# Performance work log

Hardware: AMD Instinct MI355X
Metric: run time of the kernel (lower is better)

Reference implementation:

```python
import jax, jax.numpy as jnp
import numpy as np

B, TQ, TV = 4, 256, 256
H, D, U = 512, 512, 256  # hidden_size, value_size, units


def setup_inputs() -> dict:
    key = jax.random.key(0)
    ks = jax.random.split(key, 8)
    s = 0.02
    return {
        "query": jax.random.normal(ks[0], (B, TQ, H), dtype=jnp.float32),
        "values": jax.random.normal(ks[1], (B, TV, D), dtype=jnp.float32),
        "W1": jax.random.normal(ks[2], (H, U), dtype=jnp.float32) * s,
        "b1": jnp.zeros((U,), dtype=jnp.float32),
        "W2": jax.random.normal(ks[3], (D, U), dtype=jnp.float32) * s,
        "b2": jnp.zeros((U,), dtype=jnp.float32),
        "V": jax.random.normal(ks[4], (U, 1), dtype=jnp.float32) * s,
        "bV": jnp.zeros((1,), dtype=jnp.float32),
    }


def reference(query, values, W1, b1, W2, b2, V, bV):
    # query: [B,Tq,H]  values: [B,Tv,D]
    q = jnp.einsum("bqh,hu->bqu", query, W1) + b1          # [B,Tq,U]
    v = jnp.einsum("bvd,du->bvu", values, W2) + b2          # [B,Tv,U]
    # tf.repeat over Tq is just a broadcast of v; same math without materializing repeats twice
    hidden = jnp.tanh(q[:, :, None, :] + v[:, None, :, :])  # [B,Tq,Tv,U]
    score = jnp.einsum("bqvu,u->bqv", hidden, V[:, 0]) + bV[0]  # [B,Tq,Tv]
    attn = jax.nn.softmax(score, axis=2)                    # softmax over Tv (axis=2 of score)
    context = jnp.einsum("bqv,bvd->bqd", attn, values)      # [B,Tq,D]
    return context, attn[..., None]                          # weights returned as [B,Tq,Tv,1] like TF
```

## Files before the change

### kernel.cpp

```cpp
#include <hip/hip_runtime.h>
#include <math.h>


typedef float f4 __attribute__((ext_vector_type(4)));
typedef float f2 __attribute__((ext_vector_type(2)));
typedef __attribute__((ext_vector_type(8))) short s8v;
typedef __attribute__((ext_vector_type(4))) unsigned short u4v;

#define B_    4
#define TQ_   256
#define TV_   256
#define D_    512
#define U_    256
#define KDIM  512
#define MROWS 1024

#define C2LOG2E 2.8853900817779268f

#define EQ_OFF  0
#define EVT_OFF 262144

#if __has_builtin(__builtin_amdgcn_exp2f)
#define EXP2F(x) __builtin_amdgcn_exp2f(x)
#else
#define EXP2F(x) exp2f(x)
#endif
#if __has_builtin(__builtin_amdgcn_rcpf)
#define RCPF(x) __builtin_amdgcn_rcpf(x)
#else
#define RCPF(x) (1.0f / (x))
#endif

__device__ __forceinline__ unsigned short f2bf(float f) {
    union { float f; unsigned u; } v; v.f = f;
    return (unsigned short)((v.u + 0x7FFF + ((v.u >> 16) & 1)) >> 16);
}

__global__ __launch_bounds__(256) void proj_mfma(
    const float* __restrict__ query, const float* __restrict__ values,
    const float* __restrict__ W1, const float* __restrict__ b1,
    const float* __restrict__ W2, const float* __restrict__ b2,
    float* __restrict__ ws)
{
    __shared__ unsigned short Al[2][32][40];
    __shared__ unsigned short Bl[2][32][40];

    const int tid  = threadIdx.x;
    const int proj = blockIdx.y;
    const int x    = blockIdx.x;

    int m0, n0;
    if (proj == 0) { m0 = (x >> 3) * 32; n0 = (x & 7) * 32; }
    else           { m0 = (x & 7) * 32;  n0 = (x >> 3) * 32; }

    const int drow = tid >> 3;
    const int dk   = (tid & 7) * 4;
    const int tcol = drow;
    const int tk   = dk;

    const float* dptr = (proj ? values + (size_t)(n0 + drow) * KDIM
                              : query  + (size_t)(m0 + drow) * KDIM) + dk;
    const float* tptr = (proj ? W2 + (m0 + tcol) : W1 + (n0 + tcol))
                        + (size_t)tk * U_;

    f4 d0;
    float tv0, tv1, tv2, tv3;

#define LOADR(S)                                                        \
    do {                                                                \
        d0 = *(const f4*)(dptr + (size_t)(S) * 32);                     \
        const float* tp = tptr + (size_t)(S) * 32 * U_;                 \
        tv0 = tp[0]; tv1 = tp[U_]; tv2 = tp[2 * U_]; tv3 = tp[3 * U_];  \
    } while (0)

#define WRITEB(BUF)                                                     \
    do {                                                                \
        u4v dd, tt;                                                     \
        dd[0] = f2bf(d0[0]); dd[1] = f2bf(d0[1]);                       \
        dd[2] = f2bf(d0[2]); dd[3] = f2bf(d0[3]);                       \
        tt[0] = f2bf(tv0);   tt[1] = f2bf(tv1);                         \
        tt[2] = f2bf(tv2);   tt[3] = f2bf(tv3);                         \
        unsigned short* ddst = proj ? &Bl[BUF][drow][dk] : &Al[BUF][drow][dk]; \
        unsigned short* tdst = proj ? &Al[BUF][tcol][tk] : &Bl[BUF][tcol][tk]; \
        *(u4v*)ddst = dd;                                               \
        *(u4v*)tdst = tt;                                               \
    } while (0)

    f4 acc = {};

    const int w    = tid >> 6;
    const int l    = tid & 63;
    const int fr   = l & 15;
    const int fk   = (l >> 4) * 8;
    const int band = (w & 1) * 16;
    const int colh = (w >> 1) * 16;

    LOADR(0);
    WRITEB(0);

    for (int s = 0; s < 16; ++s) {
        __syncthreads();
        if (s + 1 < 16) LOADR(s + 1);
        {
            const int bu = s & 1;
            s8v af = *(const s8v*)&Al[bu][band + fr][fk];
            s8v bf = *(const s8v*)&Bl[bu][colh + fr][fk];
            acc = __builtin_amdgcn_mfma_f32_16x16x32_bf16(af, bf, acc, 0, 0, 0);
        }
        if (s + 1 < 16) WRITEB((s + 1) & 1);
    }
#undef LOADR
#undef WRITEB

    const int orow = m0 + band + (l >> 4) * 4;
    const int ocol = n0 + colh + (l & 15);

    if (proj == 0) {
        float* E = ws + EQ_OFF;
        const float bias = b1[ocol];
        #pragma unroll
        for (int r = 0; r < 4; ++r)
            E[(size_t)(orow + r) * U_ + ocol] =
                EXP2F((acc[r] + bias) * C2LOG2E);
    } else {
        float* E = ws + EVT_OFF;
        #pragma unroll
        for (int r = 0; r < 4; ++r)
            E[(size_t)(orow + r) * MROWS + ocol] =
                EXP2F((acc[r] + b2[orow + r]) * C2LOG2E);
    }
}

__global__ __launch_bounds__(256) void score_softmax(
    const float* __restrict__ Vw, const float* __restrict__ ws,
    float* __restrict__ out)
{
    __shared__ float redmin[4][2];
    __shared__ float redsum[4][2];

    const int tid = threadIdx.x;
    const int b  = blockIdx.y;
    const int q0 = blockIdx.x * 2;

    const float* eq0 = ws + EQ_OFF + (size_t)(b * TQ_ + q0) * U_;
    const float* eq1 = eq0 + U_;
    const float* evp = ws + EVT_OFF + (size_t)b * TV_ + tid;
    float* attn = out + (size_t)B_ * TQ_ * D_ + (size_t)(b * TQ_ + q0) * TV_;

    float evA[8], evB[8];
    #pragma unroll
    for (int i = 0; i < 8; ++i) evA[i] = evp[(size_t)i * MROWS];

    f2 p = {0.f, 0.f};
    const f2 one = {1.0f, 1.0f};

#define SGRP(BUF, G)                                                    \
    _Pragma("unroll")                                                   \
    for (int i = 0; i < 8; ++i) {                                       \
        const int u = (G) * 8 + i;                                      \
        f2 eq = {eq0[u], eq1[u]};                      \
        f2 ev2 = {BUF[i], BUF[i]};                                      \
        f2 den = eq * ev2 + one;                      \
        f2 r = {RCPF(den.x), RCPF(den.y)};                              \
        f2 wv = {Vw[u], Vw[u]};                             \
        p = wv * r + p;                               \
    }

    #pragma unroll
    for (int g = 0; g < 32; g += 2) {
        #pragma unroll
        for (int i = 0; i < 8; ++i)
            evB[i] = evp[(size_t)((g + 1) * 8 + i) * MROWS];
        SGRP(evA, g)
        if (g + 2 < 32) {
            #pragma unroll
            for (int i = 0; i < 8; ++i)
                evA[i] = evp[(size_t)((g + 2) * 8 + i) * MROWS];
        }
        SGRP(evB, g + 1)
    }
#undef SGRP

    const int w = tid >> 6, lane = tid & 63;
    float m0 = p.x, m1 = p.y;
    #pragma unroll
    for (int off = 32; off; off >>= 1) {
        m0 = fminf(m0, __shfl_xor(m0, off));
        m1 = fminf(m1, __shfl_xor(m1, off));
    }
    if (lane == 0) { redmin[w][0] = m0; redmin[w][1] = m1; }
    __syncthreads();
    m0 = fminf(fminf(redmin[0][0], redmin[1][0]),
               fminf(redmin[2][0], redmin[3][0]));
    m1 = fminf(fminf(redmin[0][1], redmin[1][1]),
               fminf(redmin[2][1], redmin[3][1]));

    float e0 = EXP2F((m0 - p.x) * C2LOG2E);
    float e1 = EXP2F((m1 - p.y) * C2LOG2E);

    float s0 = e0, s1 = e1;
    #pragma unroll
    for (int off = 32; off; off >>= 1) {
        s0 += __shfl_xor(s0, off);
        s1 += __shfl_xor(s1, off);
    }
    if (lane == 0) { redsum[w][0] = s0; redsum[w][1] = s1; }
    __syncthreads();
    s0 = redsum[0][0] + redsum[1][0] + redsum[2][0] + redsum[3][0];
    s1 = redsum[0][1] + redsum[1][1] + redsum[2][1] + redsum[3][1];

    attn[tid]       = e0 * (1.0f / s0);
    attn[TV_ + tid] = e1 * (1.0f / s1);
}

__global__ __launch_bounds__(256) void ctx_mfma(
    const float* __restrict__ values, float* __restrict__ out)
{
    __shared__ unsigned short Al[2][32][40];
    __shared__ unsigned short Bl[2][32][40];

    const int tid = threadIdx.x;
    const int b   = blockIdx.y;
    const int x   = blockIdx.x;
    const int m0  = (x >> 4) * 32;
    const int n0  = (x & 15) * 32;

    const int drow = tid >> 3;
    const int dk   = (tid & 7) * 4;

    const float* attn = out + (size_t)B_ * TQ_ * D_ + (size_t)b * TQ_ * TV_;
    const float* valb = values + (size_t)b * TV_ * D_;

    const float* dptr = attn + (size_t)(m0 + drow) * TV_ + dk;
    const float* tptr = valb + (n0 + drow) + (size_t)dk * D_;

    f4 d0;
    float tv0, tv1, tv2, tv3;

#define LOADC(S)                                                        \
    do {                                                                \
        d0 = *(const f4*)(dptr + (size_t)(S) * 32);                     \
        const float* tp = tptr + (size_t)(S) * 32 * D_;                 \
        tv0 = tp[0]; tv1 = tp[D_]; tv2 = tp[2 * D_]; tv3 = tp[3 * D_];  \
    } while (0)

#define WRITEC(BUF)                                                     \
    do {                                                                \
        u4v dd, tt;                                                     \
        dd[0] = f2bf(d0[0]); dd[1] = f2bf(d0[1]);                       \
        dd[2] = f2bf(d0[2]); dd[3] = f2bf(d0[3]);                       \
        tt[0] = f2bf(tv0);   tt[1] = f2bf(tv1);                         \
        tt[2] = f2bf(tv2);   tt[3] = f2bf(tv3);                         \
        *(u4v*)&Al[BUF][drow][dk] = dd;                                 \
        *(u4v*)&Bl[BUF][drow][dk] = tt;                                 \
    } while (0)

    f4 acc = {};

    const int w    = tid >> 6;
    const int l    = tid & 63;
    const int fr   = l & 15;
    const int fk   = (l >> 4) * 8;
    const int band = (w & 1) * 16;
    const int colh = (w >> 1) * 16;

    LOADC(0);
    WRITEC(0);

    for (int s = 0; s < 8; ++s) {
        __syncthreads();
        if (s + 1 < 8) LOADC(s + 1);
        {
            const int bu = s & 1;
            s8v af = *(const s8v*)&Al[bu][band + fr][fk];
            s8v bf = *(const s8v*)&Bl[bu][colh + fr][fk];
            acc = __builtin_amdgcn_mfma_f32_16x16x32_bf16(af, bf, acc, 0, 0, 0);
        }
        if (s + 1 < 8) WRITEC((s + 1) & 1);
    }
#undef LOADC
#undef WRITEC

    const int orow = m0 + band + (l >> 4) * 4;
    const int ocol = n0 + colh + (l & 15);
    float* C = out + (size_t)b * TQ_ * D_;

    #pragma unroll
    for (int r = 0; r < 4; ++r)
        C[(size_t)(orow + r) * D_ + ocol] = acc[r];
}

extern "C" void kernel_launch(void* const* d_in, const int* in_sizes, int n_in,
                              void* d_out, int out_size, void* d_ws, size_t ws_size,
                              hipStream_t stream) {
    const float* query  = (const float*)d_in[0];
    const float* values = (const float*)d_in[1];
    const float* W1     = (const float*)d_in[2];
    const float* b1     = (const float*)d_in[3];
    const float* W2     = (const float*)d_in[4];
    const float* b2     = (const float*)d_in[5];
    const float* Vw     = (const float*)d_in[6];
    float* out = (float*)d_out;
    float* ws  = (float*)d_ws;

    proj_mfma<<<dim3(256, 2), 256, 0, stream>>>(query, values, W1, b1, W2, b2, ws);
    score_softmax<<<dim3(TQ_ / 2, B_), 256, 0, stream>>>(Vw, ws, out);
    ctx_mfma<<<dim3(128, B_), 256, 0, stream>>>(values, out);
}
```

Baseline: 40.78 us.

## Precompute bf16 transposed values and bf16 attention for context GEMM

Adds a third job to the projection kernel that writes values transposed into workspace as bf16. It also stores the exp(2v) projection as bf16, and has the softmax kernel write a bf16 copy of the attention weights. The context GEMM then loads contiguous 16-byte bf16 vectors with a 64-wide K step, instead of strided fp32 loads with per-element conversion. This removes uncoalesced column reads and conversion work from the context kernel, at the cost of extra workspace writes, an extra grid slice, and reduced precision on the exp(v) intermediate.

```diff
diff --git a/kernel.cpp b/kernel.cpp
--- a/kernel.cpp
+++ b/kernel.cpp
@@ -6,6 +6,7 @@
 typedef float f2 __attribute__((ext_vector_type(2)));
 typedef __attribute__((ext_vector_type(8))) short s8v;
 typedef __attribute__((ext_vector_type(4))) unsigned short u4v;
+typedef __attribute__((ext_vector_type(8))) unsigned short u8v;
 
 #define B_    4
 #define TQ_   256
@@ -17,8 +18,9 @@
 
 #define C2LOG2E 2.8853900817779268f
 
-#define EQ_OFF  0
-#define EVT_OFF 262144
+#define EVT_U16_OFF   524288
+#define ATTN_U16_OFF  786432
+#define VALT_U16_OFF 1048576
 
 #if __has_builtin(__builtin_amdgcn_exp2f)
 #define EXP2F(x) __builtin_amdgcn_exp2f(x)
@@ -35,6 +37,10 @@
     union { float f; unsigned u; } v; v.f = f;
     return (unsigned short)((v.u + 0x7FFF + ((v.u >> 16) & 1)) >> 16);
 }
+__device__ __forceinline__ float bf2f(unsigned short h) {
+    union { unsigned u; float f; } v; v.u = (unsigned)h << 16;
+    return v.f;
+}
 
 __global__ __launch_bounds__(256) void proj_mfma(
     const float* __restrict__ query, const float* __restrict__ values,
@@ -42,11 +48,27 @@
     const float* __restrict__ W2, const float* __restrict__ b2,
     float* __restrict__ ws)
 {
+    const int tid = threadIdx.x;
+    const int job = blockIdx.y;
+
+    if (job == 2) {
+        const int idx = blockIdx.x * 256 + tid;
+        const int d   = idx & 511;
+        const int vg  = (idx >> 9) & 31;
+        const int b   = idx >> 14;
+        const float* src = values + ((size_t)b * TV_ + vg * 8) * KDIM + d;
+        unsigned short* valT = (unsigned short*)ws + VALT_U16_OFF;
+        u8v o;
+        #pragma unroll
+        for (int j = 0; j < 8; ++j) o[j] = f2bf(src[(size_t)j * KDIM]);
+        *(u8v*)(valT + ((size_t)b * D_ + d) * TV_ + vg * 8) = o;
+        return;
+    }
+
     __shared__ unsigned short Al[2][32][40];
     __shared__ unsigned short Bl[2][32][40];
 
-    const int tid  = threadIdx.x;
-    const int proj = blockIdx.y;
+    const int proj = job;
     const int x    = blockIdx.x;
 
     int m0, n0;
@@ -116,23 +138,23 @@
     const int ocol = n0 + colh + (l & 15);
 
     if (proj == 0) {
-        float* E = ws + EQ_OFF;
+        float* E = ws;
         const float bias = b1[ocol];
         #pragma unroll
         for (int r = 0; r < 4; ++r)
             E[(size_t)(orow + r) * U_ + ocol] =
                 EXP2F((acc[r] + bias) * C2LOG2E);
     } else {
-        float* E = ws + EVT_OFF;
+        unsigned short* E = (unsigned short*)ws + EVT_U16_OFF;
         #pragma unroll
         for (int r = 0; r < 4; ++r)
             E[(size_t)(orow + r) * MROWS + ocol] =
-                EXP2F((acc[r] + b2[orow + r]) * C2LOG2E);
+                f2bf(EXP2F((acc[r] + b2[orow + r]) * C2LOG2E));
     }
 }
 
 __global__ __launch_bounds__(256) void score_softmax(
-    const float* __restrict__ Vw, const float* __restrict__ ws,
+    const float* __restrict__ Vw, float* __restrict__ ws,
     float* __restrict__ out)
 {
     __shared__ float redmin[4][2];
@@ -142,14 +164,17 @@
     const int b  = blockIdx.y;
     const int q0 = blockIdx.x * 2;
 
-    const float* eq0 = ws + EQ_OFF + (size_t)(b * TQ_ + q0) * U_;
+    const float* eq0 = ws + (size_t)(b * TQ_ + q0) * U_;
     const float* eq1 = eq0 + U_;
-    const float* evp = ws + EVT_OFF + (size_t)b * TV_ + tid;
+    const unsigned short* evp =
+        (const unsigned short*)ws + EVT_U16_OFF + (size_t)b * TV_ + tid;
     float* attn = out + (size_t)B_ * TQ_ * D_ + (size_t)(b * TQ_ + q0) * TV_;
+    unsigned short* attnbf =
+        (unsigned short*)ws + ATTN_U16_OFF + (size_t)(b * TQ_ + q0) * TV_;
 
     float evA[8], evB[8];
     #pragma unroll
-    for (int i = 0; i < 8; ++i) evA[i] = evp[(size_t)i * MROWS];
+    for (int i = 0; i < 8; ++i) evA[i] = bf2f(evp[(size_t)i * MROWS]);
 
     f2 p = {0.f, 0.f};
     const f2 one = {1.0f, 1.0f};
@@ -170,12 +195,12 @@
     for (int g = 0; g < 32; g += 2) {
         #pragma unroll
         for (int i = 0; i < 8; ++i)
-            evB[i] = evp[(size_t)((g + 1) * 8 + i) * MROWS];
+            evB[i] = bf2f(evp[(size_t)((g + 1) * 8 + i) * MROWS]);
         SGRP(evA, g)
         if (g + 2 < 32) {
             #pragma unroll
             for (int i = 0; i < 8; ++i)
-                evA[i] = evp[(size_t)((g + 2) * 8 + i) * MROWS];
+                evA[i] = bf2f(evp[(size_t)((g + 2) * 8 + i) * MROWS]);
         }
         SGRP(evB, g + 1)
     }
@@ -209,15 +234,19 @@
     s0 = redsum[0][0] + redsum[1][0] + redsum[2][0] + redsum[3][0];
     s1 = redsum[0][1] + redsum[1][1] + redsum[2][1] + redsum[3][1];
 
-    attn[tid]       = e0 * (1.0f / s0);
-    attn[TV_ + tid] = e1 * (1.0f / s1);
+    const float a0 = e0 * (1.0f / s0);
+    const float a1 = e1 * (1.0f / s1);
+    attn[tid]        = a0;
+    attn[TV_ + tid]  = a1;
+    attnbf[tid]        = f2bf(a0);
+    attnbf[TV_ + tid]  = f2bf(a1);
 }
 
 __global__ __launch_bounds__(256) void ctx_mfma(
-    const float* __restrict__ values, float* __restrict__ out)
+    const float* __restrict__ ws_ro, float* __restrict__ out)
 {
-    __shared__ unsigned short Al[2][32][40];
-    __shared__ unsigned short Bl[2][32][40];
+    __shared__ unsigned short Al[2][32][72];
+    __shared__ unsigned short Bl[2][32][72];
 
     const int tid = threadIdx.x;
     const int b   = blockIdx.y;
@@ -225,34 +254,31 @@
     const int m0  = (x >> 4) * 32;
     const int n0  = (x & 15) * 32;
 
-    const int drow = tid >> 3;
-    const int dk   = (tid & 7) * 4;
-
-    const float* attn = out + (size_t)B_ * TQ_ * D_ + (size_t)b * TQ_ * TV_;
-    const float* valb = values + (size_t)b * TV_ * D_;
-
-    const float* dptr = attn + (size_t)(m0 + drow) * TV_ + dk;
-    const float* tptr = valb + (n0 + drow) + (size_t)dk * D_;
-
-    f4 d0;
-    float tv0, tv1, tv2, tv3;
+    const int row  = tid >> 3;
+    const int koff = (tid & 7) * 8;
+
+    const unsigned short* attnbf =
+        (const unsigned short*)ws_ro + ATTN_U16_OFF;
+    const unsigned short* valT =
+        (const unsigned short*)ws_ro + VALT_U16_OFF;
+
+    const unsigned short* asrc =
+        attnbf + ((size_t)(b * TQ_ + m0 + row)) * TV_ + koff;
+    const unsigned short* bsrc =
+        valT + ((size_t)(b * D_ + n0 + row)) * TV_ + koff;
+
+    u8v a8, b8;
 
 #define LOADC(S)                                                        \
     do {                                                                \
-        d0 = *(const f4*)(dptr + (size_t)(S) * 32);                     \
-        const float* tp = tptr + (size_t)(S) * 32 * D_;                 \
-        tv0 = tp[0]; tv1 = tp[D_]; tv2 = tp[2 * D_]; tv3 = tp[3 * D_];  \
+        a8 = *(const u8v*)(asrc + (S) * 64);                            \
+        b8 = *(const u8v*)(bsrc + (S) * 64);                            \
     } while (0)
 
 #define WRITEC(BUF)                                                     \
     do {                                                                \
-        u4v dd, tt;                                                     \
-        dd[0] = f2bf(d0[0]); dd[1] = f2bf(d0[1]);                       \
-        dd[2] = f2bf(d0[2]); dd[3] = f2bf(d0[3]);                       \
-        tt[0] = f2bf(tv0);   tt[1] = f2bf(tv1);                         \
-        tt[2] = f2bf(tv2);   tt[3] = f2bf(tv3);                         \
-        *(u4v*)&Al[BUF][drow][dk] = dd;                                 \
-        *(u4v*)&Bl[BUF][drow][dk] = tt;                                 \
+        *(u8v*)&Al[BUF][row][koff] = a8;                                \
+        *(u8v*)&Bl[BUF][row][koff] = b8;                                \
     } while (0)
 
     f4 acc = {};
@@ -267,16 +293,19 @@
     LOADC(0);
     WRITEC(0);
 
-    for (int s = 0; s < 8; ++s) {
+    for (int s = 0; s < 4; ++s) {
         __syncthreads();
-        if (s + 1 < 8) LOADC(s + 1);
+        if (s + 1 < 4) LOADC(s + 1);
         {
             const int bu = s & 1;
-            s8v af = *(const s8v*)&Al[bu][band + fr][fk];
-            s8v bf = *(const s8v*)&Bl[bu][colh + fr][fk];
-            acc = __builtin_amdgcn_mfma_f32_16x16x32_bf16(af, bf, acc, 0, 0, 0);
+            s8v af0 = *(const s8v*)&Al[bu][band + fr][fk];
+            s8v af1 = *(const s8v*)&Al[bu][band + fr][fk + 32];
+            s8v bf0 = *(const s8v*)&Bl[bu][colh + fr][fk];
+            s8v bf1 = *(const s8v*)&Bl[bu][colh + fr][fk + 32];
+            acc = __builtin_amdgcn_mfma_f32_16x16x32_bf16(af0, bf0, acc, 0, 0, 0);
+            acc = __builtin_amdgcn_mfma_f32_16x16x32_bf16(af1, bf1, acc, 0, 0, 0);
         }
-        if (s + 1 < 8) WRITEC((s + 1) & 1);
+        if (s + 1 < 4) WRITEC((s + 1) & 1);
     }
 #undef LOADC
 #undef WRITEC
@@ -303,7 +332,7 @@
     float* out = (float*)d_out;
     float* ws  = (float*)d_ws;
 
-    proj_mfma<<<dim3(256, 2), 256, 0, stream>>>(query, values, W1, b1, W2, b2, ws);
+    proj_mfma<<<dim3(256, 3), 256, 0, stream>>>(query, values, W1, b1, W2, b2, ws);
     score_softmax<<<dim3(TQ_ / 2, B_), 256, 0, stream>>>(Vw, ws, out);
-    ctx_mfma<<<dim3(128, B_), 256, 0, stream>>>(values, out);
-}
+    ctx_mfma<<<dim3(128, B_), 256, 0, stream>>>(ws, out);
+}
```

After: 38.79 us. 4.9% less time.
